# Kernel tuning notes

Hardware: AMD Instinct MI355X
Metric: run time of the kernel (lower is better)

Reference implementation:

```python
import jax, jax.numpy as jnp
import numpy as np

N, C, A, E, D_OUT = 50000, 4, 16, 800000, 64
GEO_DIM = 2 * C + 9  # zero bond angles + zero dihedrals + 9 local-frame feats


def setup_inputs() -> dict:
    key = jax.random.key(0)
    ks = jax.random.split(key, 6)
    coord = jax.random.normal(ks[0], (N, C, 3), dtype=jnp.float32)
    attr = jax.random.normal(ks[1], (N, C, A), dtype=jnp.float32)
    channel_weights = jax.random.uniform(ks[2], (N, C), dtype=jnp.float32)
    W = jax.random.normal(ks[3], (D_OUT, A * A + GEO_DIM), dtype=jnp.float32) * (1.0 / np.sqrt(A * A + GEO_DIM))
    b = jnp.zeros((D_OUT,), dtype=jnp.float32)
    row = jax.random.randint(ks[4], (E,), 0, N, dtype=jnp.int32)
    col = jax.random.randint(ks[5], (E,), 0, N, dtype=jnp.int32)
    return {"coord": coord, "attr": attr, "channel_weights": channel_weights, "W": W, "b": b, "row": row, "col": col}


def _local_frames(coord):
    # coord: [N, C, 3] with channels (ca, c, n, ...) -> [N, 9] flattened rotation matrix
    ca, c, n = coord[:, 0], coord[:, 1], coord[:, 2]
    x = c - ca
    x = x / (jnp.linalg.norm(x, axis=-1, keepdims=True) + 1e-8)
    ty = n - ca
    y = ty - jnp.sum(ty * x, axis=-1, keepdims=True) * x
    y = y / (jnp.linalg.norm(y, axis=-1, keepdims=True) + 1e-8)
    z = jnp.cross(x, y)
    # torch.stack([x,y,z], dim=-1).reshape(N,-1): columns are x,y,z
    return jnp.stack([x, y, z], axis=-1).reshape(coord.shape[0], 9)


def reference(coord, attr, channel_weights, W, b, row, col):
    n_nodes, n_ch = coord.shape[0], coord.shape[1]
    n_edge = row.shape[0]
    # --- per-edge channel-pair distances, masked by channel-weight outer product ---
    diff = coord[row][:, :, None, :] - coord[col][:, None, :, :]        # [E, C, C, 3]
    coord_msg = jnp.linalg.norm(diff, axis=-1)                          # [E, C, C]
    coord_msg = coord_msg * (channel_weights[row][:, :, None] * channel_weights[col][:, None, :])
    # --- bilinear attr contraction: attr[row]^T @ coord_msg @ attr[col] ---
    radial = jnp.einsum('eia,eij,ejb->eab', attr[row], coord_msg, attr[col])  # [E, A, A]
    radial = radial.reshape(n_edge, -1)                                  # [E, A*A]
    # --- SE3 geometric features (bond/dihedral angles are zeros in source) ---
    lf = _local_frames(coord)                                            # [N, 9]
    # local_features repeated over channels; (lf[row]+lf[col]).mean over channel == lf[row]+lf[col]
    edge_lf = lf[row] + lf[col]                                          # [E, 9]
    geo = jnp.concatenate([jnp.zeros((n_edge, 2 * n_ch), radial.dtype), edge_lf], axis=-1)
    expanded = jnp.concatenate([radial, geo], axis=-1)                   # [E, A*A + GEO_DIM]
    # non-rbf path: linear_map(expanded) / (||expanded|| + CONSTANT)
    rnorm = jnp.linalg.norm(expanded, axis=-1, keepdims=True) + 1.0
    radials = (expanded @ W.T + b) / rnorm                               # [E, D_OUT]
    # --- coord_diff: row coords minus channel-mask-pooled col coords ---
    mask = (channel_weights != 0).astype(coord.dtype)                    # [N, C]
    csum = mask.sum(-1)                                                  # [N]
    pooled_col = (coord[col] * mask[col][..., None]).sum(1) / csum[col][:, None]  # [E, 3]
    coord_diff = coord[row] - pooled_col[:, None, :]                     # [E, C, 3]
    # --- node scatter-reduce: segment_sum of radials, segment_mean of coord_diff ---
    agg = jax.ops.segment_sum(radials, row, num_segments=n_nodes)        # [N, D_OUT]
    cnt = jax.ops.segment_sum(jnp.ones((n_edge,), coord.dtype), row, num_segments=n_nodes)
    coord_agg = jax.ops.segment_sum(coord_diff, row, num_segments=n_nodes) / jnp.clip(cnt, 1.0)[:, None, None]
    return jnp.concatenate([agg, coord_agg.reshape(n_nodes, -1)], axis=-1)  # [N, D_OUT + C*3]
```

## Files before the change

### kernel.cpp

```cpp
#include <hip/hip_runtime.h>
#include <math.h>

#define NN 50000
#define EDG 800000
#define OUTC 76
#define NKB 68
#define NB  196

#define CCW_OFF  0
#define LFP_OFF  (CCW_OFF + NN*16)
#define WK_OFF   (LFP_OFF + NN*16)
#define CNT_OFF  (WK_OFF + NKB*256)
#define OFFS_OFF (CNT_OFF + NN)
#define PERM_OFF (OFFS_OFF + NN + 4)
#define ECOL_OFF (PERM_OFF + EDG)
#define BSUM_OFF (ECOL_OFF + EDG)

__global__ void prep_kernel(const float* __restrict__ coord,
                            const float* __restrict__ cw,
                            const float* __restrict__ W,
                            float* __restrict__ ccwp,
                            float* __restrict__ lfp,
                            float* __restrict__ wk) {
    int t = blockIdx.x * blockDim.x + threadIdx.x;

    if (t < NKB * 64) {
        int kb = t >> 6, d = t & 63;
        float tmp[4];
        #pragma unroll
        for (int km = 0; km < 4; ++km) {
            int k = kb * 4 + km;
            int kcol = (k < 256) ? k : ((k < 265) ? k + 8 : -1);
            tmp[km] = (kcol >= 0) ? W[d * 273 + kcol] : 0.f;
        }
        ((float4*)wk)[t] = make_float4(tmp[0], tmp[1], tmp[2], tmp[3]);
    }

    if (t >= NN) return;
    const float* cp = coord + (size_t)t * 12;
    float c0x = cp[0], c0y = cp[1], c0z = cp[2];
    float c1x = cp[3], c1y = cp[4], c1z = cp[5];
    float c2x = cp[6], c2y = cp[7], c2z = cp[8];
    float c3x = cp[9], c3y = cp[10], c3z = cp[11];
    const float* wv = cw + (size_t)t * 4;
    float w0 = wv[0], w1 = wv[1], w2 = wv[2], w3 = wv[3];

    float* cc = ccwp + (size_t)t * 16;
    cc[0] = c0x; cc[1] = c0y; cc[2] = c0z; cc[3] = w0;
    cc[4] = c1x; cc[5] = c1y; cc[6] = c1z; cc[7] = w1;
    cc[8] = c2x; cc[9] = c2y; cc[10] = c2z; cc[11] = w2;
    cc[12] = c3x; cc[13] = c3y; cc[14] = c3z; cc[15] = w3;

    float xx = c1x - c0x, xy = c1y - c0y, xz = c1z - c0z;
    float invx = 1.0f / (sqrtf(xx * xx + xy * xy + xz * xz) + 1e-8f);
    xx *= invx; xy *= invx; xz *= invx;
    float tx = c2x - c0x, ty = c2y - c0y, tz = c2z - c0z;
    float dp = tx * xx + ty * xy + tz * xz;
    float yx = tx - dp * xx, yy = ty - dp * xy, yz = tz - dp * xz;
    float invy = 1.0f / (sqrtf(yx * yx + yy * yy + yz * yz) + 1e-8f);
    yx *= invy; yy *= invy; yz *= invy;
    float zx = xy * yz - xz * yy;
    float zy = xz * yx - xx * yz;
    float zz = xx * yy - xy * yx;

    float m0 = (w0 != 0.f) ? 1.f : 0.f;
    float m1 = (w1 != 0.f) ? 1.f : 0.f;
    float m2 = (w2 != 0.f) ? 1.f : 0.f;
    float m3 = (w3 != 0.f) ? 1.f : 0.f;
    float cs = m0 + m1 + m2 + m3;
    float px = (c0x * m0 + c1x * m1 + c2x * m2 + c3x * m3) / cs;
    float py = (c0y * m0 + c1y * m1 + c2y * m2 + c3y * m3) / cs;
    float pz = (c0z * m0 + c1z * m1 + c2z * m2 + c3z * m3) / cs;

    float* lp = lfp + (size_t)t * 16;
    lp[0] = xx; lp[1] = yx; lp[2] = zx;
    lp[3] = xy; lp[4] = yy; lp[5] = zy;
    lp[6] = xz; lp[7] = yz; lp[8] = zz;
    lp[9] = 0.f; lp[10] = 0.f; lp[11] = 0.f;
    lp[12] = px; lp[13] = py; lp[14] = pz; lp[15] = 0.f;
}

__global__ void hist_kernel(const int* __restrict__ row, int* __restrict__ counts,
                            int* __restrict__ perm, int E) {
    int e = blockIdx.x * blockDim.x + threadIdx.x;
    if (e < E) perm[e] = atomicAdd(&counts[row[e]], 1);
}

__global__ void scan1_kernel(const int* __restrict__ counts, int* __restrict__ bsum) {
    int t = blockIdx.x * 256 + threadIdx.x;
    int v = (t < NN) ? counts[t] : 0;
    #pragma unroll
    for (int d = 1; d < 64; d <<= 1) v += __shfl_xor(v, d);
    __shared__ int wsum[4];
    int wid = threadIdx.x >> 6, lane = threadIdx.x & 63;
    if (lane == 0) wsum[wid] = v;
    __syncthreads();
    if (threadIdx.x == 0) bsum[blockIdx.x] = wsum[0] + wsum[1] + wsum[2] + wsum[3];
}

__global__ void scan2_kernel(int* __restrict__ bsum, int* __restrict__ offs) {
    __shared__ int sh[256];
    int t = threadIdx.x;
    int v = (t < NB) ? bsum[t] : 0;
    sh[t] = v;
    __syncthreads();
    for (int d = 1; d < 256; d <<= 1) {
        int u = (t >= d) ? sh[t - d] : 0;
        __syncthreads();
        sh[t] += u;
        __syncthreads();
    }
    if (t < NB) bsum[t] = sh[t] - v;
    if (t == NB - 1) offs[NN] = sh[t];
}

__global__ void scan3_kernel(const int* __restrict__ counts, const int* __restrict__ bsum,
                             int* __restrict__ offs) {
    int t = blockIdx.x * 256 + threadIdx.x;
    int v = (t < NN) ? counts[t] : 0;
    int lane = threadIdx.x & 63, wid = threadIdx.x >> 6;
    int x = v;
    #pragma unroll
    for (int d = 1; d < 64; d <<= 1) {
        int u = __shfl_up(x, d);
        x += (lane >= d) ? u : 0;
    }
    __shared__ int wtot[4];
    if (lane == 63) wtot[wid] = x;
    __syncthreads();
    int wbase = 0;
    for (int i = 0; i < wid; ++i) wbase += wtot[i];
    if (t < NN) offs[t] = bsum[blockIdx.x] + wbase + x - v;
}

__global__ void scatter_kernel(const int* __restrict__ row, const int* __restrict__ col,
                               const int* __restrict__ offs, const int* __restrict__ perm,
                               int* __restrict__ ecol, int E) {
    int e = blockIdx.x * blockDim.x + threadIdx.x;
    if (e >= E) return;
    ecol[offs[row[e]] + perm[e]] = col[e];
}

__device__ __forceinline__ float wave_sum64(float x) {
    float v = x, t;
    t = __int_as_float(__builtin_amdgcn_update_dpp(0, __float_as_int(v), 0x111, 0xf, 0xf, true)); v += t;
    t = __int_as_float(__builtin_amdgcn_update_dpp(0, __float_as_int(v), 0x112, 0xf, 0xf, true)); v += t;
    t = __int_as_float(__builtin_amdgcn_update_dpp(0, __float_as_int(v), 0x114, 0xf, 0xf, true)); v += t;
    t = __int_as_float(__builtin_amdgcn_update_dpp(0, __float_as_int(v), 0x118, 0xf, 0xf, true)); v += t;
    t = __int_as_float(__builtin_amdgcn_update_dpp(0, __float_as_int(v), 0x142, 0xa, 0xf, true)); v += t;
    t = __int_as_float(__builtin_amdgcn_update_dpp(0, __float_as_int(v), 0x143, 0xc, 0xf, true)); v += t;
    return __int_as_float(__builtin_amdgcn_readlane(__float_as_int(v), 63));
}

#define RLF(v, k) __int_as_float(__builtin_amdgcn_readlane(__float_as_int(v), k))

__global__ __launch_bounds__(256) void edge_kernel(
    const float* __restrict__ coord, const float* __restrict__ attr,
    const float* __restrict__ bvec,
    const float* __restrict__ ccw, const float* __restrict__ lfp,
    const float* __restrict__ wk,
    const int* __restrict__ offs, const int* __restrict__ ecol,
    float* __restrict__ out) {
    __shared__ float Acbuf[4][64];
    __shared__ float S[4][280];

    const int w = threadIdx.x >> 6;
    const int l = threadIdx.x & 63;
    const int n = blockIdx.x * 4 + w;

    const int st = offs[n], en = offs[n + 1];
    const int b0 = (l & 3) * 4;
    const int i4 = (l >> 2) & 3;
    const int j4 = l & 3;
    const int a  = l >> 2;

    const float ArA0 = attr[(size_t)n * 64 + 0 * 16 + a];
    const float ArA1 = attr[(size_t)n * 64 + 1 * 16 + a];
    const float ArA2 = attr[(size_t)n * 64 + 2 * 16 + a];
    const float ArA3 = attr[(size_t)n * 64 + 3 * 16 + a];
    const float4 cown = ((const float4*)ccw)[n * 4 + i4];
    const float crx = cown.x, cry = cown.y, crz = cown.z, cwr = cown.w;
    const float lrv = lfp[(size_t)n * 16 + l];
    const float lfmask = (l < 9) ? 1.f : 0.f;
    const float pmask  = (l >= 12 && l < 15) ? 1.f : 0.f;

    float ax = 0.f, ay = 0.f, az = 0.f, aw = 0.f;
    float sgeo = 0.f, invs = 0.f, sp = 0.f;

    const float4* CCW4 = (const float4*)ccw;

    for (int base = st; base < en; base += 64) {
        int bcnt = en - base; bcnt = bcnt > 64 ? 64 : bcnt;
        int idx = base + (l < bcnt ? l : bcnt - 1);
        int cvec = ecol[idx];

        int c = __builtin_amdgcn_readlane(cvec, 0);
        float4 cc  = CCW4[c * 4 + j4];
        float  acv = attr[(size_t)c * 64 + l];
        float  lcv = lfp[c * 16 + l];

        for (int k = 0; k < bcnt; ++k) {
            Acbuf[w][l] = acv;

            int kn = (k + 1 < bcnt) ? k + 1 : k;
            int c2 = __builtin_amdgcn_readlane(cvec, kn);
            float4 cc_n  = CCW4[c2 * 4 + j4];
            float  ac_n  = attr[(size_t)c2 * 64 + l];
            float  lcv_n = lfp[c2 * 16 + l];

            float dx = crx - cc.x, dy = cry - cc.y, dz = crz - cc.z;
            float m = __builtin_amdgcn_sqrtf(dx * dx + dy * dy + dz * dz) * cwr * cc.w;

            float sm0 = RLF(m, 0),  sm1 = RLF(m, 1),  sm2 = RLF(m, 2),  sm3 = RLF(m, 3);
            float sm4 = RLF(m, 4),  sm5 = RLF(m, 5),  sm6 = RLF(m, 6),  sm7 = RLF(m, 7);
            float sm8 = RLF(m, 8),  sm9 = RLF(m, 9),  sm10 = RLF(m, 10), sm11 = RLF(m, 11);
            float sm12 = RLF(m, 12), sm13 = RLF(m, 13), sm14 = RLF(m, 14), sm15 = RLF(m, 15);

            float Ux = fmaf(ArA3, sm12, fmaf(ArA2, sm8,  fmaf(ArA1, sm4,  ArA0 * sm0)));
            float Uy = fmaf(ArA3, sm13, fmaf(ArA2, sm9,  fmaf(ArA1, sm5,  ArA0 * sm1)));
            float Uz = fmaf(ArA3, sm14, fmaf(ArA2, sm10, fmaf(ArA1, sm6,  ArA0 * sm2)));
            float Uw = fmaf(ArA3, sm15, fmaf(ArA2, sm11, fmaf(ArA1, sm7,  ArA0 * sm3)));

            float4 A0 = *(const float4*)&Acbuf[w][b0];
            float4 A1 = *(const float4*)&Acbuf[w][16 + b0];
            float4 A2 = *(const float4*)&Acbuf[w][32 + b0];
            float4 A3 = *(const float4*)&Acbuf[w][48 + b0];
            float ex = Ux * A0.x + Uy * A1.x + Uz * A2.x + Uw * A3.x;
            float ey = Ux * A0.y + Uy * A1.y + Uz * A2.y + Uw * A3.y;
            float ez = Ux * A0.z + Uy * A1.z + Uz * A2.z + Uw * A3.z;
            float ew = Ux * A0.w + Uy * A1.w + Uz * A2.w + Uw * A3.w;

            float glf  = (lrv + lcv) * lfmask;
            float part = ex * ex + ey * ey + ez * ez + ew * ew + glf * glf;
            float tot  = wave_sum64(part);
            float invr = __builtin_amdgcn_rcpf(__builtin_amdgcn_sqrtf(tot) + 1.f);

            ax = fmaf(ex, invr, ax); ay = fmaf(ey, invr, ay);
            az = fmaf(ez, invr, az); aw = fmaf(ew, invr, aw);
            sgeo = fmaf(glf, invr, sgeo);
            invs += invr;
            sp = fmaf(lcv, pmask, sp);

            cc = cc_n; acv = ac_n; lcv = lcv_n;
        }
    }

    *(float4*)&S[w][l * 4] = make_float4(ax, ay, az, aw);
    if (l < 9)       S[w][256 + l] = sgeo;
    else if (l < 16) S[w][256 + l] = 0.f;
    if (l == 16)     S[w][272] = invs;
    if (l >= 12 && l < 15) S[w][273 + (l - 12)] = sp;
    if (l == 17)     S[w][276] = (float)(en - st);

    float invsum = S[w][272];
    float acc = bvec[l] * invsum;
    const float4* WK4 = (const float4*)wk;
    #pragma unroll 4
    for (int kb = 0; kb < NKB; ++kb) {
        float4 wv = WK4[kb * 64 + l];
        float4 sv = *(const float4*)&S[w][kb * 4];
        acc += wv.x * sv.x + wv.y * sv.y + wv.z * sv.z + wv.w * sv.w;
    }
    out[(size_t)n * OUTC + l] = acc;

    float cntv = S[w][276];
    float invc = __builtin_amdgcn_rcpf(fmaxf(cntv, 1.f));
    if (l < 12) {
        int x = l % 3;
        out[(size_t)n * OUTC + 64 + l] = (cntv * coord[(size_t)n * 12 + l] - S[w][273 + x]) * invc;
    }
}

extern "C" void kernel_launch(void* const* d_in, const int* in_sizes, int n_in,
                              void* d_out, int out_size, void* d_ws, size_t ws_size,
                              hipStream_t stream) {
    const float* coord = (const float*)d_in[0];
    const float* attr  = (const float*)d_in[1];
    const float* cw    = (const float*)d_in[2];
    const float* W     = (const float*)d_in[3];
    const float* bvec  = (const float*)d_in[4];
    const int*   row   = (const int*)d_in[5];
    const int*   col   = (const int*)d_in[6];
    float* out = (float*)d_out;
    float* ws  = (float*)d_ws;
    int E = in_sizes[5];

    float* ccwp = ws + CCW_OFF;
    float* lfp  = ws + LFP_OFF;
    float* wk   = ws + WK_OFF;
    int* counts = (int*)(ws + CNT_OFF);
    int* offs   = (int*)(ws + OFFS_OFF);
    int* perm   = (int*)(ws + PERM_OFF);
    int* ecol   = (int*)(ws + ECOL_OFF);
    int* bsum   = (int*)(ws + BSUM_OFF);

    hipMemsetAsync(counts, 0, NN * sizeof(int), stream);
    prep_kernel<<<(NN + 255) / 256, 256, 0, stream>>>(coord, cw, W, ccwp, lfp, wk);
    hist_kernel<<<(E + 255) / 256, 256, 0, stream>>>(row, counts, perm, E);
    scan1_kernel<<<NB, 256, 0, stream>>>(counts, bsum);
    scan2_kernel<<<1, 256, 0, stream>>>(bsum, offs);
    scan3_kernel<<<NB, 256, 0, stream>>>(counts, bsum, offs);
    scatter_kernel<<<(E + 255) / 256, 256, 0, stream>>>(row, col, offs, perm, ecol, E);
    edge_kernel<<<NN / 4, 256, 0, stream>>>(coord, attr, bvec, ccwp, lfp, wk,
                                            offs, ecol, out);
}
```

Baseline: 324.6 us.

## Fuse prep with histogram, atomic-cursor scan, and swizzle-based edge contraction

Merges the node prep and edge histogram into one launch and replaces the three-pass prefix scan with a single pass that reserves each block's base via an atomic cursor. Segments are therefore non-monotonic in node order, so each node's end comes from its count rather than the next offset. In the edge loop, the LDS staging of the neighbour's attributes and the 16 readlanes of the distance mask give way to direct float4 global loads of attr, ds_swizzle broadcasts and quad DPP permutes. It also adds a launch-bounds occupancy hint. The new loads raise register pressure and redundant global traffic in exchange for fewer launches and less LDS and readlane work.

```diff
diff --git a/kernel.cpp b/kernel.cpp
--- a/kernel.cpp
+++ b/kernel.cpp
@@ -11,18 +11,23 @@
 #define LFP_OFF  (CCW_OFF + NN*16)
 #define WK_OFF   (LFP_OFF + NN*16)
 #define CNT_OFF  (WK_OFF + NKB*256)
-#define OFFS_OFF (CNT_OFF + NN)
-#define PERM_OFF (OFFS_OFF + NN + 4)
+#define CUR_OFF  (CNT_OFF + NN)
+#define OFFS_OFF (CUR_OFF + 4)
+#define PERM_OFF (OFFS_OFF + NN)
 #define ECOL_OFF (PERM_OFF + EDG)
-#define BSUM_OFF (ECOL_OFF + EDG)
-
-__global__ void prep_kernel(const float* __restrict__ coord,
-                            const float* __restrict__ cw,
-                            const float* __restrict__ W,
-                            float* __restrict__ ccwp,
-                            float* __restrict__ lfp,
-                            float* __restrict__ wk) {
+
+__global__ void prep_hist_kernel(const float* __restrict__ coord,
+                                 const float* __restrict__ cw,
+                                 const float* __restrict__ W,
+                                 const int* __restrict__ row,
+                                 float* __restrict__ ccwp,
+                                 float* __restrict__ lfp,
+                                 float* __restrict__ wk,
+                                 int* __restrict__ counts,
+                                 int* __restrict__ perm, int E) {
     int t = blockIdx.x * blockDim.x + threadIdx.x;
+
+    if (t < E) perm[t] = atomicAdd(&counts[row[t]], 1);
 
     if (t < NKB * 64) {
         int kb = t >> 6, d = t & 63;
@@ -80,42 +85,9 @@
     lp[12] = px; lp[13] = py; lp[14] = pz; lp[15] = 0.f;
 }
 
-__global__ void hist_kernel(const int* __restrict__ row, int* __restrict__ counts,
-                            int* __restrict__ perm, int E) {
-    int e = blockIdx.x * blockDim.x + threadIdx.x;
-    if (e < E) perm[e] = atomicAdd(&counts[row[e]], 1);
-}
-
-__global__ void scan1_kernel(const int* __restrict__ counts, int* __restrict__ bsum) {
-    int t = blockIdx.x * 256 + threadIdx.x;
-    int v = (t < NN) ? counts[t] : 0;
-    #pragma unroll
-    for (int d = 1; d < 64; d <<= 1) v += __shfl_xor(v, d);
-    __shared__ int wsum[4];
-    int wid = threadIdx.x >> 6, lane = threadIdx.x & 63;
-    if (lane == 0) wsum[wid] = v;
-    __syncthreads();
-    if (threadIdx.x == 0) bsum[blockIdx.x] = wsum[0] + wsum[1] + wsum[2] + wsum[3];
-}
-
-__global__ void scan2_kernel(int* __restrict__ bsum, int* __restrict__ offs) {
-    __shared__ int sh[256];
-    int t = threadIdx.x;
-    int v = (t < NB) ? bsum[t] : 0;
-    sh[t] = v;
-    __syncthreads();
-    for (int d = 1; d < 256; d <<= 1) {
-        int u = (t >= d) ? sh[t - d] : 0;
-        __syncthreads();
-        sh[t] += u;
-        __syncthreads();
-    }
-    if (t < NB) bsum[t] = sh[t] - v;
-    if (t == NB - 1) offs[NN] = sh[t];
-}
-
-__global__ void scan3_kernel(const int* __restrict__ counts, const int* __restrict__ bsum,
-                             int* __restrict__ offs) {
+__global__ void scanalloc_kernel(const int* __restrict__ counts,
+                                 int* __restrict__ cursor,
+                                 int* __restrict__ offs) {
     int t = blockIdx.x * 256 + threadIdx.x;
     int v = (t < NN) ? counts[t] : 0;
     int lane = threadIdx.x & 63, wid = threadIdx.x >> 6;
@@ -126,11 +98,15 @@
         x += (lane >= d) ? u : 0;
     }
     __shared__ int wtot[4];
+    __shared__ int sbase;
     if (lane == 63) wtot[wid] = x;
+    __syncthreads();
+    if (threadIdx.x == 0)
+        sbase = atomicAdd(cursor, wtot[0] + wtot[1] + wtot[2] + wtot[3]);
     __syncthreads();
     int wbase = 0;
     for (int i = 0; i < wid; ++i) wbase += wtot[i];
-    if (t < NN) offs[t] = bsum[blockIdx.x] + wbase + x - v;
+    if (t < NN) offs[t] = sbase + wbase + x - v;
 }
 
 __global__ void scatter_kernel(const int* __restrict__ row, const int* __restrict__ col,
@@ -152,23 +128,27 @@
     return __int_as_float(__builtin_amdgcn_readlane(__float_as_int(v), 63));
 }
 
-#define RLF(v, k) __int_as_float(__builtin_amdgcn_readlane(__float_as_int(v), k))
-
-__global__ __launch_bounds__(256) void edge_kernel(
+#define SWZ(x, pat) __int_as_float(__builtin_amdgcn_ds_swizzle(__float_as_int(x), pat))
+#define QPERM(x, pat) __int_as_float(__builtin_amdgcn_update_dpp(0, __float_as_int(x), pat, 0xf, 0xf, true))
+
+__global__ __launch_bounds__(256, 6) void edge_kernel(
     const float* __restrict__ coord, const float* __restrict__ attr,
     const float* __restrict__ bvec,
     const float* __restrict__ ccw, const float* __restrict__ lfp,
     const float* __restrict__ wk,
-    const int* __restrict__ offs, const int* __restrict__ ecol,
+    const int* __restrict__ offs, const int* __restrict__ counts,
+    const int* __restrict__ ecol,
     float* __restrict__ out) {
-    __shared__ float Acbuf[4][64];
     __shared__ float S[4][280];
 
     const int w = threadIdx.x >> 6;
     const int l = threadIdx.x & 63;
+    const int l15 = l & 15;
     const int n = blockIdx.x * 4 + w;
 
-    const int st = offs[n], en = offs[n + 1];
+    const int st = offs[n];
+    const int deg = counts[n];
+    const int en = st + deg;
     const int b0 = (l & 3) * 4;
     const int i4 = (l >> 2) & 3;
     const int j4 = l & 3;
@@ -180,7 +160,7 @@
     const float ArA3 = attr[(size_t)n * 64 + 3 * 16 + a];
     const float4 cown = ((const float4*)ccw)[n * 4 + i4];
     const float crx = cown.x, cry = cown.y, crz = cown.z, cwr = cown.w;
-    const float lrv = lfp[(size_t)n * 16 + l];
+    const float lrv = lfp[(size_t)n * 16 + l15];
     const float lfmask = (l < 9) ? 1.f : 0.f;
     const float pmask  = (l >= 12 && l < 15) ? 1.f : 0.f;
 
@@ -195,43 +175,46 @@
         int cvec = ecol[idx];
 
         int c = __builtin_amdgcn_readlane(cvec, 0);
+        const float* ar0 = attr + (size_t)c * 64;
+        float4 A0 = *(const float4*)(ar0 + b0);
+        float4 A1 = *(const float4*)(ar0 + 16 + b0);
+        float4 A2 = *(const float4*)(ar0 + 32 + b0);
+        float4 A3 = *(const float4*)(ar0 + 48 + b0);
         float4 cc  = CCW4[c * 4 + j4];
-        float  acv = attr[(size_t)c * 64 + l];
-        float  lcv = lfp[c * 16 + l];
+        float  lcv = lfp[c * 16 + l15];
 
         for (int k = 0; k < bcnt; ++k) {
-            Acbuf[w][l] = acv;
-
             int kn = (k + 1 < bcnt) ? k + 1 : k;
             int c2 = __builtin_amdgcn_readlane(cvec, kn);
-            float4 cc_n  = CCW4[c2 * 4 + j4];
-            float  ac_n  = attr[(size_t)c2 * 64 + l];
-            float  lcv_n = lfp[c2 * 16 + l];
+            const float* arn = attr + (size_t)c2 * 64;
+            float4 An0 = *(const float4*)(arn + b0);
+            float4 An1 = *(const float4*)(arn + 16 + b0);
+            float4 An2 = *(const float4*)(arn + 32 + b0);
+            float4 An3 = *(const float4*)(arn + 48 + b0);
+            float4 ccn  = CCW4[c2 * 4 + j4];
+            float  lcvn = lfp[c2 * 16 + l15];
 
             float dx = crx - cc.x, dy = cry - cc.y, dz = crz - cc.z;
-            float m = __builtin_amdgcn_sqrtf(dx * dx + dy * dy + dz * dz) * cwr * cc.w;
-
-            float sm0 = RLF(m, 0),  sm1 = RLF(m, 1),  sm2 = RLF(m, 2),  sm3 = RLF(m, 3);
-            float sm4 = RLF(m, 4),  sm5 = RLF(m, 5),  sm6 = RLF(m, 6),  sm7 = RLF(m, 7);
-            float sm8 = RLF(m, 8),  sm9 = RLF(m, 9),  sm10 = RLF(m, 10), sm11 = RLF(m, 11);
-            float sm12 = RLF(m, 12), sm13 = RLF(m, 13), sm14 = RLF(m, 14), sm15 = RLF(m, 15);
-
-            float Ux = fmaf(ArA3, sm12, fmaf(ArA2, sm8,  fmaf(ArA1, sm4,  ArA0 * sm0)));
-            float Uy = fmaf(ArA3, sm13, fmaf(ArA2, sm9,  fmaf(ArA1, sm5,  ArA0 * sm1)));
-            float Uz = fmaf(ArA3, sm14, fmaf(ArA2, sm10, fmaf(ArA1, sm6,  ArA0 * sm2)));
-            float Uw = fmaf(ArA3, sm15, fmaf(ArA2, sm11, fmaf(ArA1, sm7,  ArA0 * sm3)));
-
-            float4 A0 = *(const float4*)&Acbuf[w][b0];
-            float4 A1 = *(const float4*)&Acbuf[w][16 + b0];
-            float4 A2 = *(const float4*)&Acbuf[w][32 + b0];
-            float4 A3 = *(const float4*)&Acbuf[w][48 + b0];
-            float ex = Ux * A0.x + Uy * A1.x + Uz * A2.x + Uw * A3.x;
-            float ey = Ux * A0.y + Uy * A1.y + Uz * A2.y + Uw * A3.y;
-            float ez = Ux * A0.z + Uy * A1.z + Uz * A2.z + Uw * A3.z;
-            float ew = Ux * A0.w + Uy * A1.w + Uz * A2.w + Uw * A3.w;
+            float m = __builtin_amdgcn_sqrtf(fmaf(dx, dx, fmaf(dy, dy, dz * dz))) * cwr * cc.w;
+
+            float M0 = SWZ(m, 0x013);
+            float M1 = SWZ(m, 0x093);
+            float M2 = SWZ(m, 0x113);
+            float M3 = SWZ(m, 0x193);
+
+            float Uo = fmaf(ArA3, M3, fmaf(ArA2, M2, fmaf(ArA1, M1, ArA0 * M0)));
+            float U0 = QPERM(Uo, 0x00);
+            float U1 = QPERM(Uo, 0x55);
+            float U2 = QPERM(Uo, 0xAA);
+            float U3 = QPERM(Uo, 0xFF);
+
+            float ex = fmaf(U3, A3.x, fmaf(U2, A2.x, fmaf(U1, A1.x, U0 * A0.x)));
+            float ey = fmaf(U3, A3.y, fmaf(U2, A2.y, fmaf(U1, A1.y, U0 * A0.y)));
+            float ez = fmaf(U3, A3.z, fmaf(U2, A2.z, fmaf(U1, A1.z, U0 * A0.z)));
+            float ew = fmaf(U3, A3.w, fmaf(U2, A2.w, fmaf(U1, A1.w, U0 * A0.w)));
 
             float glf  = (lrv + lcv) * lfmask;
-            float part = ex * ex + ey * ey + ez * ez + ew * ew + glf * glf;
+            float part = fmaf(glf, glf, fmaf(ew, ew, fmaf(ez, ez, fmaf(ey, ey, ex * ex))));
             float tot  = wave_sum64(part);
             float invr = __builtin_amdgcn_rcpf(__builtin_amdgcn_sqrtf(tot) + 1.f);
 
@@ -241,7 +224,8 @@
             invs += invr;
             sp = fmaf(lcv, pmask, sp);
 
-            cc = cc_n; acv = ac_n; lcv = lcv_n;
+            A0 = An0; A1 = An1; A2 = An2; A3 = An3;
+            cc = ccn; lcv = lcvn;
         }
     }
 
@@ -250,7 +234,6 @@
     else if (l < 16) S[w][256 + l] = 0.f;
     if (l == 16)     S[w][272] = invs;
     if (l >= 12 && l < 15) S[w][273 + (l - 12)] = sp;
-    if (l == 17)     S[w][276] = (float)(en - st);
 
     float invsum = S[w][272];
     float acc = bvec[l] * invsum;
@@ -263,7 +246,7 @@
     }
     out[(size_t)n * OUTC + l] = acc;
 
-    float cntv = S[w][276];
+    float cntv = (float)deg;
     float invc = __builtin_amdgcn_rcpf(fmaxf(cntv, 1.f));
     if (l < 12) {
         int x = l % 3;
@@ -289,18 +272,16 @@
     float* lfp  = ws + LFP_OFF;
     float* wk   = ws + WK_OFF;
     int* counts = (int*)(ws + CNT_OFF);
+    int* cursor = (int*)(ws + CUR_OFF);
     int* offs   = (int*)(ws + OFFS_OFF);
     int* perm   = (int*)(ws + PERM_OFF);
     int* ecol   = (int*)(ws + ECOL_OFF);
-    int* bsum   = (int*)(ws + BSUM_OFF);
-
-    hipMemsetAsync(counts, 0, NN * sizeof(int), stream);
-    prep_kernel<<<(NN + 255) / 256, 256, 0, stream>>>(coord, cw, W, ccwp, lfp, wk);
-    hist_kernel<<<(E + 255) / 256, 256, 0, stream>>>(row, counts, perm, E);
-    scan1_kernel<<<NB, 256, 0, stream>>>(counts, bsum);
-    scan2_kernel<<<1, 256, 0, stream>>>(bsum, offs);
-    scan3_kernel<<<NB, 256, 0, stream>>>(counts, bsum, offs);
+
+    hipMemsetAsync(counts, 0, (NN + 4) * sizeof(int), stream);
+    prep_hist_kernel<<<(E + 255) / 256, 256, 0, stream>>>(
+        coord, cw, W, row, ccwp, lfp, wk, counts, perm, E);
+    scanalloc_kernel<<<NB, 256, 0, stream>>>(counts, cursor, offs);
     scatter_kernel<<<(E + 255) / 256, 256, 0, stream>>>(row, col, offs, perm, ecol, E);
     edge_kernel<<<NN / 4, 256, 0, stream>>>(coord, attr, bvec, ccwp, lfp, wk,
-                                            offs, ecol, out);
-}
+                                            offs, counts, ecol, out);
+}
```

Measured after the change: 353.7 us. +9.0%, slower.
